# Kernel tuning notes

Hardware: AMD Instinct MI355X
Metric: run time of the kernel (lower is better)

Reference implementation:

```python
import jax, jax.numpy as jnp
import numpy as np

B, T, V, D, H, C = 128, 512, 50000, 128, 256, 10


def _lstm_scan(xs, W, U, b):
    # xs: [T, B, in]; Keras gate order i, f, g(candidate), o.
    xW = jnp.einsum('tbi,ij->tbj', xs, W) + b  # precompute input projection
    Bsz = xs.shape[1]
    Hd = U.shape[0]
    h0 = jnp.zeros((Bsz, Hd), xs.dtype)

    def step(carry, zx):
        h, c = carry
        z = zx + h @ U
        i, f, g, o = jnp.split(z, 4, axis=-1)
        i = jax.nn.sigmoid(i)
        f = jax.nn.sigmoid(f)
        g = jnp.tanh(g)
        o = jax.nn.sigmoid(o)
        c = f * c + i * g
        h = o * jnp.tanh(c)
        return (h, c), h

    (hT, _), hs = jax.lax.scan(step, (h0, h0), xW)
    return hs, hT


def setup_inputs() -> dict:
    key = jax.random.key(0)
    ks = jax.random.split(key, 16)
    f32 = jnp.float32

    def glorot(k, shape):
        fan = shape[0] + shape[1]
        return jax.random.uniform(k, shape, f32, -1.0, 1.0) * np.sqrt(6.0 / fan)

    x = jax.random.randint(ks[0], (B, T), 0, V, dtype=jnp.int32)
    emb = jax.random.normal(ks[1], (V, D), f32) * 0.05
    # layer 1: input D -> 4H per direction
    W1f = glorot(ks[2], (D, 4 * H)); U1f = glorot(ks[3], (H, 4 * H)); b1f = jnp.zeros((4 * H,), f32)
    W1b = glorot(ks[4], (D, 4 * H)); U1b = glorot(ks[5], (H, 4 * H)); b1b = jnp.zeros((4 * H,), f32)
    # layer 2: input 2H -> 4H per direction
    W2f = glorot(ks[6], (2 * H, 4 * H)); U2f = glorot(ks[7], (H, 4 * H)); b2f = jnp.zeros((4 * H,), f32)
    W2b = glorot(ks[8], (2 * H, 4 * H)); U2b = glorot(ks[9], (H, 4 * H)); b2b = jnp.zeros((4 * H,), f32)
    Wd = glorot(ks[10], (2 * H, C)); bd = jnp.zeros((C,), f32)
    return dict(x=x, emb=emb, W1f=W1f, U1f=U1f, b1f=b1f, W1b=W1b, U1b=U1b, b1b=b1b,
                W2f=W2f, U2f=U2f, b2f=b2f, W2b=W2b, U2b=U2b, b2b=b2b, Wd=Wd, bd=bd)


def reference(x, emb, W1f, U1f, b1f, W1b, U1b, b1b, W2f, U2f, b2f, W2b, U2b, b2b, Wd, bd):
    # Embedding lookup -> [T, B, D] (time-major for scan). Dropout is inference-off.
    e = jnp.transpose(emb[x], (1, 0, 2))
    # Bidirectional LSTM 1 (return_sequences)
    hs_f, _ = _lstm_scan(e, W1f, U1f, b1f)
    hs_b, _ = _lstm_scan(e[::-1], W1b, U1b, b1b)
    seq = jnp.concatenate([hs_f, hs_b[::-1]], axis=-1)  # [T, B, 2H]
    # Bidirectional LSTM 2 (return last states)
    _, hT_f = _lstm_scan(seq, W2f, U2f, b2f)
    _, hT_b = _lstm_scan(seq[::-1], W2b, U2b, b2b)
    h = jnp.concatenate([hT_f, hT_b], axis=-1)  # [B, 2H]
    return jax.nn.softmax(h @ Wd + bd, axis=-1)
```

## Files before the change

### kernel.cpp

```cpp
#include <hip/hip_runtime.h>
#include <hip/hip_bf16.h>

#define B_ 128
#define T_ 512
#define H_ 256
#define G4_ 1024
#define D_ 128

typedef short s8v   __attribute__((ext_vector_type(8)));
typedef float f32x4 __attribute__((ext_vector_type(4)));
typedef unsigned short u16x4 __attribute__((ext_vector_type(4)));
typedef unsigned short u16x8 __attribute__((ext_vector_type(8)));
typedef unsigned int   u32x4 __attribute__((ext_vector_type(4)));
typedef unsigned short ush;
typedef unsigned long long ull;

#define BAR_LDS() asm volatile("s_waitcnt lgkmcnt(0)\n\ts_barrier" ::: "memory")

__device__ __forceinline__ void xstore(ull* p, ull v) {
  (void)__hip_atomic_exchange(p, v, __ATOMIC_RELAXED, __HIP_MEMORY_SCOPE_AGENT);
}
__device__ __forceinline__ ull xload(const ull* p) {
  return __hip_atomic_load(p, __ATOMIC_RELAXED, __HIP_MEMORY_SCOPE_AGENT);
}

__device__ __align__(256) ush   g_xw[(size_t)T_ * 2 * B_ * G4_];
__device__ __align__(256) ush   g_hseq[(size_t)T_ * B_ * 512];
__device__ __align__(256) ull   g_hx2[16 * 2 * 2 * 2 * 512];
__device__ __align__(256) float g_hT[B_ * 512];
__device__ __align__(256) unsigned g_tcnt[512];
__device__ __align__(256) ush   g_wtall[2359296];

__device__ __forceinline__ ush f2b(float f) {
  unsigned u = __builtin_bit_cast(unsigned, f);
  u += 0x7FFFu + ((u >> 16) & 1u);
  return (ush)(u >> 16);
}
__device__ __forceinline__ float b2f(ush h) {
  unsigned u = ((unsigned)h) << 16;
  return __builtin_bit_cast(float, u);
}
__device__ __forceinline__ float sigm(float x) {
  x = fminf(15.f, fmaxf(-15.f, x));
  return 1.f / (1.f + __expf(-x));
}
__device__ __forceinline__ float tanh_(float x) {
  x = fminf(8.f, fmaxf(-8.f, x));
  float e = __expf(-2.f * x);
  return (1.f - e) / (1.f + e);
}

__global__ __launch_bounds__(256, 4) void prep_w(
    const float* __restrict__ Wf, const float* __restrict__ Wb,
    ush* __restrict__ WTf, ush* __restrict__ WTb, int K)
{
  __shared__ ush tile[64][65];
  const float* W = blockIdx.z ? Wb : Wf;
  ush* WT = blockIdx.z ? WTb : WTf;
  int nt = blockIdx.x & 15, kt = blockIdx.x >> 4;
  int tid = threadIdx.x;
  for (int i = tid; i < 4096; i += 256) {
    int k = i >> 6, n = i & 63;
    tile[k][n] = f2b(W[(size_t)(kt * 64 + k) * 1024 + nt * 64 + n]);
  }
  __syncthreads();
  for (int i = tid; i < 4096; i += 256) {
    int n = i >> 6, k = i & 63;
    WT[(size_t)(nt * 64 + n) * K + kt * 64 + k] = tile[k][n];
  }
}

__global__ __launch_bounds__(512, 4) void gemm_xw(
    const int* __restrict__ xi, const float* __restrict__ emb,
    const ush* __restrict__ WTf, const ush* __restrict__ WTb)
{
  __shared__ __align__(16) ush A_lds[128 * 72];
  __shared__ __align__(16) ush BT_lds[128 * 72];
  const int tid = threadIdx.x;
  const int lane = tid & 63;
  const int w = tid >> 6;
  const int nb = blockIdx.x;
  const int t = blockIdx.y;
  const int dir = blockIdx.z;
  const ush* WT = dir ? WTb : WTf;

  const f32x4 zero4 = {0.f, 0.f, 0.f, 0.f};
  f32x4 acc[8];
#pragma unroll
  for (int i = 0; i < 8; ++i) acc[i] = zero4;

  const int rowA0 = tid >> 3;
  const int ccA = tid & 7;
  int idx0 = xi[rowA0 * T_ + t];
  int idx1 = xi[(rowA0 + 64) * T_ + t];

  for (int kc = 0; kc < 2; ++kc) {
    __syncthreads();
    {
      const float* s = emb + (size_t)idx0 * D_ + kc * 64 + ccA * 8;
      f32x4 a = *(const f32x4*)s;
      f32x4 b = *(const f32x4*)(s + 4);
      u16x8 v;
      v[0]=f2b(a[0]); v[1]=f2b(a[1]); v[2]=f2b(a[2]); v[3]=f2b(a[3]);
      v[4]=f2b(b[0]); v[5]=f2b(b[1]); v[6]=f2b(b[2]); v[7]=f2b(b[3]);
      *(u16x8*)&A_lds[rowA0 * 72 + ccA * 8] = v;
    }
    {
      const float* s = emb + (size_t)idx1 * D_ + kc * 64 + ccA * 8;
      f32x4 a = *(const f32x4*)s;
      f32x4 b = *(const f32x4*)(s + 4);
      u16x8 v;
      v[0]=f2b(a[0]); v[1]=f2b(a[1]); v[2]=f2b(a[2]); v[3]=f2b(a[3]);
      v[4]=f2b(b[0]); v[5]=f2b(b[1]); v[6]=f2b(b[2]); v[7]=f2b(b[3]);
      *(u16x8*)&A_lds[(rowA0 + 64) * 72 + ccA * 8] = v;
    }
    {
      int n = tid >> 2, k8 = (tid & 3) * 2;
      const ush* src = WT + (size_t)(nb * 128 + n) * 128 + kc * 64 + k8 * 8;
      *(u32x4*)&BT_lds[n * 72 + k8 * 8] = *(const u32x4*)src;
      *(u32x4*)&BT_lds[n * 72 + k8 * 8 + 8] = *(const u32x4*)(src + 8);
    }
    __syncthreads();
#pragma unroll
    for (int kt = 0; kt < 2; ++kt) {
      const int koff = kt * 32 + ((lane >> 4) << 3);
      s8v af = *(const s8v*)&A_lds[(w * 16 + (lane & 15)) * 72 + koff];
#pragma unroll
      for (int nt = 0; nt < 8; ++nt) {
        s8v bf = *(const s8v*)&BT_lds[(nt * 16 + (lane & 15)) * 72 + koff];
        acc[nt] = __builtin_amdgcn_mfma_f32_16x16x32_bf16(af, bf, acc[nt], 0, 0, 0);
      }
    }
  }
  ush* dst = g_xw + ((size_t)t * 2 + dir) * ((size_t)B_ * G4_);
#pragma unroll
  for (int nt = 0; nt < 8; ++nt) {
    int colg = nb * 128 + nt * 16 + (lane & 15);
    int g = colg >> 8, hc = colg & 255;
#pragma unroll
    for (int jj = 0; jj < 4; ++jj) {
      int row = w * 16 + ((lane >> 4) << 2) + jj;
      dst[(size_t)row * 1024 + hc * 4 + g] = f2b(acc[nt][jj]);
    }
  }
}

__global__ __launch_bounds__(512, 2) void mega(
    int layer, const ush* __restrict__ UTf, const ush* __restrict__ UTb,
    const float* __restrict__ bfp, const float* __restrict__ bbp,
    int writeSeq, int ngemm,
    const ush* __restrict__ WT2f, const ush* __restrict__ WT2b)
{
  __shared__ __align__(16) ush smem[2 * 128 * 72];
  const int bx = blockIdx.x;
  const int tid = threadIdx.x;
  const int lane = tid & 63;
  const int w = tid >> 6;
  const int l15 = lane & 15;
  const int lq = lane >> 4;

  if (bx < 64) {
    const int slice = bx & 15;
    const int dir = (bx >> 4) & 1;
    const int nh = bx >> 5;
    const ush* UT = dir ? UTb : UTf;
    const float* bias = dir ? bbp : bfp;
    const int mycol = nh * 128 + w * 16 + l15;
    const int rowb = slice * 8;
    const unsigned sbase = (unsigned)(layer * T_);
    ush* h0 = smem;

    s8v bfr[4][8];
#pragma unroll
    for (int g = 0; g < 4; ++g) {
      const ush* up = UT + (size_t)(g * 256 + mycol) * 256;
#pragma unroll
      for (int kt = 0; kt < 8; ++kt)
        bfr[g][kt] = *(const s8v*)(up + kt * 32 + lq * 8);
    }
    float bias_r[4];
#pragma unroll
    for (int g = 0; g < 4; ++g) bias_r[g] = bias[g * 256 + mycol];

    {
      ull* z = (ull*)smem;
      z[tid] = 0ull; z[tid + 512] = 0ull; z[tid + 1024] = 0ull; z[tid + 1536] = 0ull;
    }
    __syncthreads();

    float c_[4] = {0.f, 0.f, 0.f, 0.f};
    ull* hx_sd = g_hx2 + (size_t)(slice * 2 + dir) * 2048;

    const int w_src = tid >> 6, r_ = tid & 63;
    const int blkc = r_ >> 5, lqs = (r_ >> 4) & 1, l15s = r_ & 15;
    const int col_p = (nh ^ 1) * 128 + w_src * 16 + l15s;
    const int r0c = lqs * 4 + blkc * 2;
    const int c8p = col_p >> 3, wp = col_p & 7;
    const int sw0 = ((c8p ^ r0c) & 31) * 8 + wp;
    const int sw1 = ((c8p ^ (r0c + 1)) & 31) * 8 + wp;
    const int xrow = (lq & 1) * 4;

    u16x4 xv[4];
    {
      int t0 = dir ? (T_ - 1) : 0;
      const ush* xp = g_xw + (((size_t)t0 * 2 + dir) * B_ + rowb) * 1024 + mycol * 4;
#pragma unroll
      for (int j = 0; j < 4; ++j) xv[j] = *(const u16x4*)(xp + (size_t)(xrow + j) * 1024);
    }

    for (int s = 0; s < T_; ++s) {
      const int p = s & 1;
      if (s > 0) {
        const ull* ap = hx_sd + (size_t)(p * 2 + (nh ^ 1)) * 512 + tid;
        unsigned target = sbase + (unsigned)s;
        ull v;
        for (;;) {
          v = xload(ap);
          if ((unsigned)(v >> 32) >= target) break;
          __builtin_amdgcn_s_sleep(1);
        }
        ush* dl = h0 + p * 4096;
        dl[r0c * 256 + sw0] = (ush)v;
        dl[(r0c + 1) * 256 + sw1] = (ush)(v >> 16);
      }
      BAR_LDS();
      if (writeSeq) {
        if (tid == 0 && s >= 2) {
          int td = dir ? (T_ + 1 - s) : (s - 2);
          __hip_atomic_fetch_add(&g_tcnt[td], 1u, __ATOMIC_RELAXED, __HIP_MEMORY_SCOPE_AGENT);
        }
        if (s > 0 && tid < 128) {
          int row8 = tid >> 4, idx = tid & 15;
          int col = nh * 128 + idx * 8;
          int c8 = col >> 3;
          const ush* srcl = h0 + p * 4096 + row8 * 256 + ((c8 ^ row8) & 31) * 8;
          ull lo = *(const ull*)srcl;
          ull hi = *(const ull*)(srcl + 4);
          int tprev = dir ? (T_ - s) : (s - 1);
          ull* dst = (ull*)&g_hseq[((size_t)tprev * B_ + rowb + row8) * 512 + dir * 256 + col];
          xstore(dst, lo);
          xstore(dst + 1, hi);
        }
      }
      u16x4 xn[4];
      {
        int tn = dir ? max(0, T_ - 2 - s) : min(T_ - 1, s + 1);
        const ush* xp = g_xw + (((size_t)tn * 2 + dir) * B_ + rowb) * 1024 + mycol * 4;
#pragma unroll
        for (int j = 0; j < 4; ++j) xn[j] = *(const u16x4*)(xp + (size_t)(xrow + j) * 1024);
      }
      s8v af[8];
#pragma unroll
      for (int kt = 0; kt < 8; ++kt) {
        int c8 = kt * 4 + lq;
        af[kt] = *(const s8v*)(h0 + p * 4096 + l15 * 256 + ((c8 ^ l15) & 31) * 8);
      }
      f32x4 acc[4];
      const f32x4 zero4 = {0.f, 0.f, 0.f, 0.f};
#pragma unroll
      for (int g = 0; g < 4; ++g) acc[g] = zero4;
#pragma unroll
      for (int kt = 0; kt < 8; ++kt) {
#pragma unroll
        for (int g = 0; g < 4; ++g)
          acc[g] = __builtin_amdgcn_mfma_f32_16x16x32_bf16(af[kt], bfr[g][kt], acc[g], 0, 0, 0);
      }
      ush hv[4];
#pragma unroll
      for (int j = 0; j < 4; ++j) {
        float vi = acc[0][j] + b2f(xv[j][0]) + bias_r[0];
        float vf = acc[1][j] + b2f(xv[j][1]) + bias_r[1];
        float vg = acc[2][j] + b2f(xv[j][2]) + bias_r[2];
        float vo = acc[3][j] + b2f(xv[j][3]) + bias_r[3];
        float ig = sigm(vi), fg = sigm(vf), gg = tanh_(vg), og = sigm(vo);
        float cc = fg * c_[j] + ig * gg;
        c_[j] = cc;
        hv[j] = f2b(og * tanh_(cc));
      }
      if (lq < 2 && s + 1 < T_) {
        ull seqw = ((ull)(sbase + (unsigned)s + 1u)) << 32;
        ull e0 = (ull)hv[0] | ((ull)hv[1] << 16) | seqw;
        ull e1 = (ull)hv[2] | ((ull)hv[3] << 16) | seqw;
        ull* ep = hx_sd + (size_t)((p ^ 1) * 2 + nh) * 512 + w * 64 + lq * 16 + l15;
        xstore(ep, e0);
        xstore(ep + 32, e1);
      }
      if (lq < 2) {
        int c8o = mycol >> 3, wo = mycol & 7;
        ush* dl = h0 + (p ^ 1) * 4096;
#pragma unroll
        for (int j = 0; j < 4; ++j) {
          int r = lq * 4 + j;
          dl[r * 256 + (((c8o ^ r) & 31) * 8 + wo)] = hv[j];
        }
      }
#pragma unroll
      for (int j = 0; j < 4; ++j) xv[j] = xn[j];
    }
    __syncthreads();
    const ush* bufl = h0 + (T_ & 1) * 4096;
    if (writeSeq) {
      if (tid < 128) {
        int row8 = tid >> 4, idx = tid & 15;
        int col = nh * 128 + idx * 8;
        int c8 = col >> 3;
        const ush* srcl = bufl + row8 * 256 + ((c8 ^ row8) & 31) * 8;
        ull lo = *(const ull*)srcl;
        ull hi = *(const ull*)(srcl + 4);
        int tlast = dir ? 0 : (T_ - 1);
        ull* dst = (ull*)&g_hseq[((size_t)tlast * B_ + rowb + row8) * 512 + dir * 256 + col];
        xstore(dst, lo);
        xstore(dst + 1, hi);
      }
      asm volatile("s_waitcnt vmcnt(0)" ::: "memory");
      __syncthreads();
      if (tid == 0) {
        int ta = dir ? 1 : (T_ - 2);
        int tb2 = dir ? 0 : (T_ - 1);
        __hip_atomic_fetch_add(&g_tcnt[ta], 1u, __ATOMIC_RELAXED, __HIP_MEMORY_SCOPE_AGENT);
        __hip_atomic_fetch_add(&g_tcnt[tb2], 1u, __ATOMIC_RELAXED, __HIP_MEMORY_SCOPE_AGENT);
      }
    } else {
      if (tid < 128) {
        int row8 = tid >> 4, idx = tid & 15;
        int col = nh * 128 + idx * 8;
        int c8 = col >> 3;
        const ush* srcl = bufl + row8 * 256 + ((c8 ^ row8) & 31) * 8;
        float* dstf = g_hT + (size_t)(rowb + row8) * 512 + dir * 256 + col;
        f32x4 f0, f1;
#pragma unroll
        for (int j = 0; j < 4; ++j) { f0[j] = b2f(srcl[j]); f1[j] = b2f(srcl[4 + j]); }
        *(f32x4*)dstf = f0;
        *(f32x4*)(dstf + 4) = f1;
      }
    }
  } else {
    if (ngemm <= 0) return;
    ush* A_lds = smem;
    ush* BT_lds = smem + 128 * 72;
    const int wg = bx - 64;
    const int rowA0 = tid >> 3;
    const int ccA = tid & 7;

    for (int u = wg; u < 8192; u += ngemm) {
      int pairIdx = u >> 4, sub = u & 15;
      int nb = sub & 7, gdir = sub >> 3;
      int t = (pairIdx & 1) ? (255 - (pairIdx >> 1)) : (256 + (pairIdx >> 1));
      const ush* WT = gdir ? WT2b : WT2f;
      for (;;) {
        unsigned v = __hip_atomic_load(&g_tcnt[t], __ATOMIC_RELAXED, __HIP_MEMORY_SCOPE_AGENT);
        if (v >= 64u) break;
        __builtin_amdgcn_s_sleep(4);
      }
      const f32x4 zero4 = {0.f, 0.f, 0.f, 0.f};
      f32x4 acc[8];
#pragma unroll
      for (int i = 0; i < 8; ++i) acc[i] = zero4;
      for (int kc = 0; kc < 8; ++kc) {
        __syncthreads();
        {
          const ush* s0 = g_hseq + ((size_t)(t * B_ + rowA0)) * 512 + kc * 64 + ccA * 8;
          *(u32x4*)&A_lds[rowA0 * 72 + ccA * 8] = *(const u32x4*)s0;
          const ush* s1 = g_hseq + ((size_t)(t * B_ + rowA0 + 64)) * 512 + kc * 64 + ccA * 8;
          *(u32x4*)&A_lds[(rowA0 + 64) * 72 + ccA * 8] = *(const u32x4*)s1;
        }
        {
          int n = tid >> 2, k8 = (tid & 3) * 2;
          const ush* src = WT + (size_t)(nb * 128 + n) * 512 + kc * 64 + k8 * 8;
          *(u32x4*)&BT_lds[n * 72 + k8 * 8] = *(const u32x4*)src;
          *(u32x4*)&BT_lds[n * 72 + k8 * 8 + 8] = *(const u32x4*)(src + 8);
        }
        __syncthreads();
#pragma unroll
        for (int kt = 0; kt < 2; ++kt) {
          const int koff = kt * 32 + (lq << 3);
          s8v af = *(const s8v*)&A_lds[(w * 16 + l15) * 72 + koff];
#pragma unroll
          for (int nt = 0; nt < 8; ++nt) {
            s8v bf = *(const s8v*)&BT_lds[(nt * 16 + l15) * 72 + koff];
            acc[nt] = __builtin_amdgcn_mfma_f32_16x16x32_bf16(af, bf, acc[nt], 0, 0, 0);
          }
        }
      }
      ush* dst = g_xw + ((size_t)t * 2 + gdir) * ((size_t)B_ * G4_);
#pragma unroll
      for (int nt = 0; nt < 8; ++nt) {
        int colg = nb * 128 + nt * 16 + l15;
        int g = colg >> 8, hc = colg & 255;
#pragma unroll
        for (int jj = 0; jj < 4; ++jj) {
          int row = w * 16 + (lq << 2) + jj;
          dst[(size_t)row * 1024 + hc * 4 + g] = f2b(acc[nt][jj]);
        }
      }
    }
  }
}

__global__ __launch_bounds__(512, 1) void dense_softmax(
    const float* __restrict__ Wd, const float* __restrict__ bd, float* __restrict__ out)
{
  __shared__ float wT[10 * 512];
  __shared__ float part[512 * 10];
  int tid = threadIdx.x;
  for (int i = tid; i < 5120; i += 512) {
    int k = i / 10, j = i - k * 10;
    wT[j * 512 + k] = Wd[i];
  }
  __syncthreads();
  int row = tid >> 2, q = tid & 3;
  float acc[10];
#pragma unroll
  for (int j = 0; j < 10; ++j) acc[j] = 0.f;
  const float* hrow = g_hT + (size_t)row * 512 + q * 128;
  for (int kk = 0; kk < 32; ++kk) {
    f32x4 h4 = *(const f32x4*)(hrow + kk * 4);
#pragma unroll
    for (int j = 0; j < 10; ++j) {
      f32x4 w4 = *(const f32x4*)&wT[j * 512 + q * 128 + kk * 4];
      acc[j] += h4[0] * w4[0] + h4[1] * w4[1] + h4[2] * w4[2] + h4[3] * w4[3];
    }
  }
#pragma unroll
  for (int j = 0; j < 10; ++j) part[tid * 10 + j] = acc[j];
  __syncthreads();
  if (tid < 128) {
    float lg[10];
#pragma unroll
    for (int j = 0; j < 10; ++j)
      lg[j] = bd[j] + part[(tid * 4 + 0) * 10 + j] + part[(tid * 4 + 1) * 10 + j]
                    + part[(tid * 4 + 2) * 10 + j] + part[(tid * 4 + 3) * 10 + j];
    float m = lg[0];
#pragma unroll
    for (int j = 1; j < 10; ++j) m = fmaxf(m, lg[j]);
    float ssum = 0.f;
#pragma unroll
    for (int j = 0; j < 10; ++j) { lg[j] = __expf(lg[j] - m); ssum += lg[j]; }
    float inv = 1.f / ssum;
#pragma unroll
    for (int j = 0; j < 10; ++j) out[tid * 10 + j] = lg[j] * inv;
  }
}

extern "C" void kernel_launch(void* const* d_in, const int* in_sizes, int n_in,
                              void* d_out, int out_size, void* d_ws, size_t ws_size,
                              hipStream_t stream) {
  (void)in_sizes; (void)n_in; (void)d_ws; (void)ws_size; (void)out_size;
  const int* x = (const int*)d_in[0];
  const float* emb = (const float*)d_in[1];
  const float* W1f = (const float*)d_in[2];
  const float* U1f = (const float*)d_in[3];
  const float* b1f = (const float*)d_in[4];
  const float* W1b = (const float*)d_in[5];
  const float* U1b = (const float*)d_in[6];
  const float* b1b = (const float*)d_in[7];
  const float* W2f = (const float*)d_in[8];
  const float* U2f = (const float*)d_in[9];
  const float* b2f = (const float*)d_in[10];
  const float* W2b = (const float*)d_in[11];
  const float* U2b = (const float*)d_in[12];
  const float* b2b = (const float*)d_in[13];
  const float* Wd  = (const float*)d_in[14];
  const float* bd  = (const float*)d_in[15];
  float* out = (float*)d_out;

  void* hx_p = nullptr; void* wt_p = nullptr; void* tc_p = nullptr;
  hipGetSymbolAddress(&hx_p, HIP_SYMBOL(g_hx2));
  hipGetSymbolAddress(&wt_p, HIP_SYMBOL(g_wtall));
  hipGetSymbolAddress(&tc_p, HIP_SYMBOL(g_tcnt));
  ush* wt = (ush*)wt_p;
  hipMemsetAsync(hx_p, 0, sizeof(ull) * 16 * 2 * 2 * 2 * 512, stream);
  hipMemsetAsync(tc_p, 0, sizeof(unsigned) * 512, stream);

  ush* wt1f = wt;                 ush* wt1b = wt1f + 131072;
  ush* ut1f = wt1b + 131072;      ush* ut1b = ut1f + 262144;
  ush* wt2f = ut1b + 262144;      ush* wt2b = wt2f + 524288;
  ush* ut2f = wt2b + 524288;      ush* ut2b = ut2f + 262144;

  prep_w<<<dim3(32, 1, 2), 256, 0, stream>>>(W1f, W1b, wt1f, wt1b, 128);
  prep_w<<<dim3(64, 1, 2), 256, 0, stream>>>(U1f, U1b, ut1f, ut1b, 256);
  prep_w<<<dim3(128, 1, 2), 256, 0, stream>>>(W2f, W2b, wt2f, wt2b, 512);
  prep_w<<<dim3(64, 1, 2), 256, 0, stream>>>(U2f, U2b, ut2f, ut2b, 256);

  gemm_xw<<<dim3(8, T_, 2), 512, 0, stream>>>(x, emb, wt1f, wt1b);
  mega<<<256, 512, 0, stream>>>(0, ut1f, ut1b, b1f, b1b, 1, 192, wt2f, wt2b);
  mega<<<64, 512, 0, stream>>>(1, ut2f, ut2b, b2f, b2b, 0, 0, nullptr, nullptr);
  dense_softmax<<<1, 512, 0, stream>>>(Wd, bd, out);
}
```

Measured before the change: 3.308 ms.

## Split recurrent matmul into own-half and partner-half to overlap with exchange

The recurrent h@U product is split by K into the half this block computed itself and the half owned by the partner block. The own-half MFMAs are issued right after the new h is written to LDS, before waiting on the partner's data, so only the partner-half remains on the critical path after the cross-block spin-wait. The next-step xW prefetch is also moved to after the gate computation. This adds an extra LDS barrier per step, and the accumulators now carry across iterations.

```diff
diff --git a/kernel.cpp b/kernel.cpp
--- a/kernel.cpp
+++ b/kernel.cpp
@@ -170,13 +170,15 @@
     const unsigned sbase = (unsigned)(layer * T_);
     ush* h0 = smem;
 
-    s8v bfr[4][8];
+    s8v bfrO[4][4], bfrP[4][4];
 #pragma unroll
     for (int g = 0; g < 4; ++g) {
       const ush* up = UT + (size_t)(g * 256 + mycol) * 256;
 #pragma unroll
-      for (int kt = 0; kt < 8; ++kt)
-        bfr[g][kt] = *(const s8v*)(up + kt * 32 + lq * 8);
+      for (int i = 0; i < 4; ++i) {
+        bfrO[g][i] = *(const s8v*)(up + (nh * 128 + i * 32) + lq * 8);
+        bfrP[g][i] = *(const s8v*)(up + ((nh ^ 1) * 128 + i * 32) + lq * 8);
+      }
     }
     float bias_r[4];
 #pragma unroll
@@ -207,6 +209,11 @@
 #pragma unroll
       for (int j = 0; j < 4; ++j) xv[j] = *(const u16x4*)(xp + (size_t)(xrow + j) * 1024);
     }
+
+    const f32x4 zero4 = {0.f, 0.f, 0.f, 0.f};
+    f32x4 acc[4];
+#pragma unroll
+    for (int g = 0; g < 4; ++g) acc[g] = zero4;
 
     for (int s = 0; s < T_; ++s) {
       const int p = s & 1;
@@ -242,28 +249,19 @@
           xstore(dst + 1, hi);
         }
       }
-      u16x4 xn[4];
       {
-        int tn = dir ? max(0, T_ - 2 - s) : min(T_ - 1, s + 1);
-        const ush* xp = g_xw + (((size_t)tn * 2 + dir) * B_ + rowb) * 1024 + mycol * 4;
-#pragma unroll
-        for (int j = 0; j < 4; ++j) xn[j] = *(const u16x4*)(xp + (size_t)(xrow + j) * 1024);
-      }
-      s8v af[8];
-#pragma unroll
-      for (int kt = 0; kt < 8; ++kt) {
-        int c8 = kt * 4 + lq;
-        af[kt] = *(const s8v*)(h0 + p * 4096 + l15 * 256 + ((c8 ^ l15) & 31) * 8);
-      }
-      f32x4 acc[4];
-      const f32x4 zero4 = {0.f, 0.f, 0.f, 0.f};
-#pragma unroll
-      for (int g = 0; g < 4; ++g) acc[g] = zero4;
-#pragma unroll
-      for (int kt = 0; kt < 8; ++kt) {
-#pragma unroll
-        for (int g = 0; g < 4; ++g)
-          acc[g] = __builtin_amdgcn_mfma_f32_16x16x32_bf16(af[kt], bfr[g][kt], acc[g], 0, 0, 0);
+        s8v afP[4];
+#pragma unroll
+        for (int i = 0; i < 4; ++i) {
+          int c8 = ((nh ^ 1) * 4 + i) * 4 + lq;
+          afP[i] = *(const s8v*)(h0 + p * 4096 + l15 * 256 + ((c8 ^ l15) & 31) * 8);
+        }
+#pragma unroll
+        for (int i = 0; i < 4; ++i) {
+#pragma unroll
+          for (int g = 0; g < 4; ++g)
+            acc[g] = __builtin_amdgcn_mfma_f32_16x16x32_bf16(afP[i], bfrP[g][i], acc[g], 0, 0, 0);
+        }
       }
       ush hv[4];
 #pragma unroll
@@ -277,6 +275,13 @@
         c_[j] = cc;
         hv[j] = f2b(og * tanh_(cc));
       }
+      u16x4 xn[4];
+      {
+        int tn = dir ? max(0, T_ - 2 - s) : min(T_ - 1, s + 1);
+        const ush* xp = g_xw + (((size_t)tn * 2 + dir) * B_ + rowb) * 1024 + mycol * 4;
+#pragma unroll
+        for (int j = 0; j < 4; ++j) xn[j] = *(const u16x4*)(xp + (size_t)(xrow + j) * 1024);
+      }
       if (lq < 2 && s + 1 < T_) {
         ull seqw = ((ull)(sbase + (unsigned)s + 1u)) << 32;
         ull e0 = (ull)hv[0] | ((ull)hv[1] << 16) | seqw;
@@ -292,6 +297,23 @@
         for (int j = 0; j < 4; ++j) {
           int r = lq * 4 + j;
           dl[r * 256 + (((c8o ^ r) & 31) * 8 + wo)] = hv[j];
+        }
+      }
+      BAR_LDS();
+#pragma unroll
+      for (int g = 0; g < 4; ++g) acc[g] = zero4;
+      {
+        s8v afO[4];
+#pragma unroll
+        for (int i = 0; i < 4; ++i) {
+          int c8 = (nh * 4 + i) * 4 + lq;
+          afO[i] = *(const s8v*)(h0 + (p ^ 1) * 4096 + l15 * 256 + ((c8 ^ l15) & 31) * 8);
+        }
+#pragma unroll
+        for (int i = 0; i < 4; ++i) {
+#pragma unroll
+          for (int g = 0; g < 4; ++g)
+            acc[g] = __builtin_amdgcn_mfma_f32_16x16x32_bf16(afO[i], bfrO[g][i], acc[g], 0, 0, 0);
         }
       }
 #pragma unroll
```

After: 3.244 ms. Within noise of the previous version (-1.9%).

## Give each recurrent block all 256 hidden columns to drop cross-block h exchange

Applied to the files above, without the earlier changes.

Recurrent blocks now use 1024 threads (16 waves) and each one owns every hidden column for 16 batch rows, so the per-step hidden state is exchanged through LDS with a single barrier. The global-memory spin-wait handshake between paired blocks and the g_hx2 buffer are removed. Blocks per layer drop from 64 to 16, the hseq writeout and completion counters are adjusted to match (pipelined one step later with a vmcnt wait), and the overlapped layer-2 input GEMM blocks are re-tiled for 16 waves. In exchange, each block holds twice the recurrent work serially, so fewer CUs run the recurrence and per-step latency may grow.

```diff
diff --git a/kernel.cpp b/kernel.cpp
--- a/kernel.cpp
+++ b/kernel.cpp
@@ -18,15 +18,11 @@
 #define BAR_LDS() asm volatile("s_waitcnt lgkmcnt(0)\n\ts_barrier" ::: "memory")
 
 __device__ __forceinline__ void xstore(ull* p, ull v) {
-  (void)__hip_atomic_exchange(p, v, __ATOMIC_RELAXED, __HIP_MEMORY_SCOPE_AGENT);
-}
-__device__ __forceinline__ ull xload(const ull* p) {
-  return __hip_atomic_load(p, __ATOMIC_RELAXED, __HIP_MEMORY_SCOPE_AGENT);
+  __hip_atomic_store(p, v, __ATOMIC_RELAXED, __HIP_MEMORY_SCOPE_AGENT);
 }
 
 __device__ __align__(256) ush   g_xw[(size_t)T_ * 2 * B_ * G4_];
 __device__ __align__(256) ush   g_hseq[(size_t)T_ * B_ * 512];
-__device__ __align__(256) ull   g_hx2[16 * 2 * 2 * 2 * 512];
 __device__ __align__(256) float g_hT[B_ * 512];
 __device__ __align__(256) unsigned g_tcnt[512];
 __device__ __align__(256) ush   g_wtall[2359296];
@@ -145,7 +141,7 @@
   }
 }
 
-__global__ __launch_bounds__(512, 2) void mega(
+__global__ __launch_bounds__(1024, 1) void mega(
     int layer, const ush* __restrict__ UTf, const ush* __restrict__ UTb,
     const float* __restrict__ bfp, const float* __restrict__ bbp,
     int writeSeq, int ngemm,
@@ -159,15 +155,13 @@
   const int l15 = lane & 15;
   const int lq = lane >> 4;
 
-  if (bx < 64) {
-    const int slice = bx & 15;
-    const int dir = (bx >> 4) & 1;
-    const int nh = bx >> 5;
+  if (bx < 16) {
+    const int slice = bx & 7;
+    const int dir = bx >> 3;
     const ush* UT = dir ? UTb : UTf;
     const float* bias = dir ? bbp : bfp;
-    const int mycol = nh * 128 + w * 16 + l15;
-    const int rowb = slice * 8;
-    const unsigned sbase = (unsigned)(layer * T_);
+    const int mycol = w * 16 + l15;
+    const int rowb = slice * 16;
     ush* h0 = smem;
 
     s8v bfr[4][8];
@@ -184,62 +178,40 @@
 
     {
       ull* z = (ull*)smem;
-      z[tid] = 0ull; z[tid + 512] = 0ull; z[tid + 1024] = 0ull; z[tid + 1536] = 0ull;
+      z[tid] = 0ull; z[tid + 1024] = 0ull;
     }
     __syncthreads();
 
     float c_[4] = {0.f, 0.f, 0.f, 0.f};
-    ull* hx_sd = g_hx2 + (size_t)(slice * 2 + dir) * 2048;
-
-    const int w_src = tid >> 6, r_ = tid & 63;
-    const int blkc = r_ >> 5, lqs = (r_ >> 4) & 1, l15s = r_ & 15;
-    const int col_p = (nh ^ 1) * 128 + w_src * 16 + l15s;
-    const int r0c = lqs * 4 + blkc * 2;
-    const int c8p = col_p >> 3, wp = col_p & 7;
-    const int sw0 = ((c8p ^ r0c) & 31) * 8 + wp;
-    const int sw1 = ((c8p ^ (r0c + 1)) & 31) * 8 + wp;
-    const int xrow = (lq & 1) * 4;
+
+    const int srow = tid >> 6;
+    const int scg = tid & 63;
+    const int sc8 = scg >> 1, swo = (scg & 1) * 4;
+    const int sswz = ((sc8 ^ srow) & 31) * 8 + swo;
 
     u16x4 xv[4];
     {
       int t0 = dir ? (T_ - 1) : 0;
       const ush* xp = g_xw + (((size_t)t0 * 2 + dir) * B_ + rowb) * 1024 + mycol * 4;
 #pragma unroll
-      for (int j = 0; j < 4; ++j) xv[j] = *(const u16x4*)(xp + (size_t)(xrow + j) * 1024);
-    }
+      for (int j = 0; j < 4; ++j) xv[j] = *(const u16x4*)(xp + (size_t)(lq * 4 + j) * 1024);
+    }
+
+    const f32x4 zero4 = {0.f, 0.f, 0.f, 0.f};
 
     for (int s = 0; s < T_; ++s) {
       const int p = s & 1;
-      if (s > 0) {
-        const ull* ap = hx_sd + (size_t)(p * 2 + (nh ^ 1)) * 512 + tid;
-        unsigned target = sbase + (unsigned)s;
-        ull v;
-        for (;;) {
-          v = xload(ap);
-          if ((unsigned)(v >> 32) >= target) break;
-          __builtin_amdgcn_s_sleep(1);
-        }
-        ush* dl = h0 + p * 4096;
-        dl[r0c * 256 + sw0] = (ush)v;
-        dl[(r0c + 1) * 256 + sw1] = (ush)(v >> 16);
-      }
-      BAR_LDS();
       if (writeSeq) {
-        if (tid == 0 && s >= 2) {
-          int td = dir ? (T_ + 1 - s) : (s - 2);
+        asm volatile("s_waitcnt vmcnt(0)" ::: "memory");
+        if (tid == 0 && s >= 3) {
+          int td = dir ? (T_ + 2 - s) : (s - 3);
           __hip_atomic_fetch_add(&g_tcnt[td], 1u, __ATOMIC_RELAXED, __HIP_MEMORY_SCOPE_AGENT);
         }
-        if (s > 0 && tid < 128) {
-          int row8 = tid >> 4, idx = tid & 15;
-          int col = nh * 128 + idx * 8;
-          int c8 = col >> 3;
-          const ush* srcl = h0 + p * 4096 + row8 * 256 + ((c8 ^ row8) & 31) * 8;
-          ull lo = *(const ull*)srcl;
-          ull hi = *(const ull*)(srcl + 4);
+        if (s > 0) {
+          const ush* srcl = h0 + p * 4096 + srow * 256 + sswz;
           int tprev = dir ? (T_ - s) : (s - 1);
-          ull* dst = (ull*)&g_hseq[((size_t)tprev * B_ + rowb + row8) * 512 + dir * 256 + col];
-          xstore(dst, lo);
-          xstore(dst + 1, hi);
+          xstore((ull*)&g_hseq[((size_t)tprev * B_ + rowb + srow) * 512 + dir * 256 + scg * 4],
+                 *(const ull*)srcl);
         }
       }
       u16x4 xn[4];
@@ -247,7 +219,7 @@
         int tn = dir ? max(0, T_ - 2 - s) : min(T_ - 1, s + 1);
         const ush* xp = g_xw + (((size_t)tn * 2 + dir) * B_ + rowb) * 1024 + mycol * 4;
 #pragma unroll
-        for (int j = 0; j < 4; ++j) xn[j] = *(const u16x4*)(xp + (size_t)(xrow + j) * 1024);
+        for (int j = 0; j < 4; ++j) xn[j] = *(const u16x4*)(xp + (size_t)(lq * 4 + j) * 1024);
       }
       s8v af[8];
 #pragma unroll
@@ -256,7 +228,6 @@
         af[kt] = *(const s8v*)(h0 + p * 4096 + l15 * 256 + ((c8 ^ l15) & 31) * 8);
       }
       f32x4 acc[4];
-      const f32x4 zero4 = {0.f, 0.f, 0.f, 0.f};
 #pragma unroll
       for (int g = 0; g < 4; ++g) acc[g] = zero4;
 #pragma unroll
@@ -277,15 +248,7 @@
         c_[j] = cc;
         hv[j] = f2b(og * tanh_(cc));
       }
-      if (lq < 2 && s + 1 < T_) {
-        ull seqw = ((ull)(sbase + (unsigned)s + 1u)) << 32;
-        ull e0 = (ull)hv[0] | ((ull)hv[1] << 16) | seqw;
-        ull e1 = (ull)hv[2] | ((ull)hv[3] << 16) | seqw;
-        ull* ep = hx_sd + (size_t)((p ^ 1) * 2 + nh) * 512 + w * 64 + lq * 16 + l15;
-        xstore(ep, e0);
-        xstore(ep + 32, e1);
-      }
-      if (lq < 2) {
+      {
         int c8o = mycol >> 3, wo = mycol & 7;
         ush* dl = h0 + (p ^ 1) * 4096;
 #pragma unroll
@@ -294,53 +257,45 @@
           dl[r * 256 + (((c8o ^ r) & 31) * 8 + wo)] = hv[j];
         }
       }
+      BAR_LDS();
 #pragma unroll
       for (int j = 0; j < 4; ++j) xv[j] = xn[j];
     }
-    __syncthreads();
     const ush* bufl = h0 + (T_ & 1) * 4096;
     if (writeSeq) {
-      if (tid < 128) {
-        int row8 = tid >> 4, idx = tid & 15;
-        int col = nh * 128 + idx * 8;
-        int c8 = col >> 3;
-        const ush* srcl = bufl + row8 * 256 + ((c8 ^ row8) & 31) * 8;
-        ull lo = *(const ull*)srcl;
-        ull hi = *(const ull*)(srcl + 4);
+      {
+        const ush* srcl = bufl + srow * 256 + sswz;
         int tlast = dir ? 0 : (T_ - 1);
-        ull* dst = (ull*)&g_hseq[((size_t)tlast * B_ + rowb + row8) * 512 + dir * 256 + col];
-        xstore(dst, lo);
-        xstore(dst + 1, hi);
+        xstore((ull*)&g_hseq[((size_t)tlast * B_ + rowb + srow) * 512 + dir * 256 + scg * 4],
+               *(const ull*)srcl);
       }
       asm volatile("s_waitcnt vmcnt(0)" ::: "memory");
       __syncthreads();
       if (tid == 0) {
-        int ta = dir ? 1 : (T_ - 2);
-        int tb2 = dir ? 0 : (T_ - 1);
+        int ta = dir ? 2 : (T_ - 3);
+        int tb = dir ? 1 : (T_ - 2);
+        int tc = dir ? 0 : (T_ - 1);
         __hip_atomic_fetch_add(&g_tcnt[ta], 1u, __ATOMIC_RELAXED, __HIP_MEMORY_SCOPE_AGENT);
-        __hip_atomic_fetch_add(&g_tcnt[tb2], 1u, __ATOMIC_RELAXED, __HIP_MEMORY_SCOPE_AGENT);
+        __hip_atomic_fetch_add(&g_tcnt[tb], 1u, __ATOMIC_RELAXED, __HIP_MEMORY_SCOPE_AGENT);
+        __hip_atomic_fetch_add(&g_tcnt[tc], 1u, __ATOMIC_RELAXED, __HIP_MEMORY_SCOPE_AGENT);
       }
     } else {
-      if (tid < 128) {
-        int row8 = tid >> 4, idx = tid & 15;
-        int col = nh * 128 + idx * 8;
-        int c8 = col >> 3;
-        const ush* srcl = bufl + row8 * 256 + ((c8 ^ row8) & 31) * 8;
-        float* dstf = g_hT + (size_t)(rowb + row8) * 512 + dir * 256 + col;
-        f32x4 f0, f1;
-#pragma unroll
-        for (int j = 0; j < 4; ++j) { f0[j] = b2f(srcl[j]); f1[j] = b2f(srcl[4 + j]); }
-        *(f32x4*)dstf = f0;
-        *(f32x4*)(dstf + 4) = f1;
-      }
+      const ush* srcl = bufl + srow * 256 + sswz;
+      float* dstf = g_hT + (size_t)(rowb + srow) * 512 + dir * 256 + scg * 4;
+      f32x4 fv;
+#pragma unroll
+      for (int j = 0; j < 4; ++j) fv[j] = b2f(srcl[j]);
+      *(f32x4*)dstf = fv;
     }
   } else {
     if (ngemm <= 0) return;
     ush* A_lds = smem;
     ush* BT_lds = smem + 128 * 72;
-    const int wg = bx - 64;
-    const int rowA0 = tid >> 3;
+    const int wg = bx - 16;
+    const int rowA = tid >> 3;
     const int ccA = tid & 7;
+    const int rs = w & 7;
+    const int ch = w >> 3;
 
     for (int u = wg; u < 8192; u += ngemm) {
       int pairIdx = u >> 4, sub = u & 15;
@@ -349,47 +304,41 @@
       const ush* WT = gdir ? WT2b : WT2f;
       for (;;) {
         unsigned v = __hip_atomic_load(&g_tcnt[t], __ATOMIC_RELAXED, __HIP_MEMORY_SCOPE_AGENT);
-        if (v >= 64u) break;
+        if (v >= 16u) break;
         __builtin_amdgcn_s_sleep(4);
       }
       const f32x4 zero4 = {0.f, 0.f, 0.f, 0.f};
-      f32x4 acc[8];
-#pragma unroll
-      for (int i = 0; i < 8; ++i) acc[i] = zero4;
+      f32x4 acc[4];
+#pragma unroll
+      for (int i = 0; i < 4; ++i) acc[i] = zero4;
       for (int kc = 0; kc < 8; ++kc) {
         __syncthreads();
         {
-          const ush* s0 = g_hseq + ((size_t)(t * B_ + rowA0)) * 512 + kc * 64 + ccA * 8;
-          *(u32x4*)&A_lds[rowA0 * 72 + ccA * 8] = *(const u32x4*)s0;
-          const ush* s1 = g_hseq + ((size_t)(t * B_ + rowA0 + 64)) * 512 + kc * 64 + ccA * 8;
-          *(u32x4*)&A_lds[(rowA0 + 64) * 72 + ccA * 8] = *(const u32x4*)s1;
-        }
-        {
-          int n = tid >> 2, k8 = (tid & 3) * 2;
-          const ush* src = WT + (size_t)(nb * 128 + n) * 512 + kc * 64 + k8 * 8;
-          *(u32x4*)&BT_lds[n * 72 + k8 * 8] = *(const u32x4*)src;
-          *(u32x4*)&BT_lds[n * 72 + k8 * 8 + 8] = *(const u32x4*)(src + 8);
+          const ush* s0 = g_hseq + ((size_t)(t * B_ + rowA)) * 512 + kc * 64 + ccA * 8;
+          *(u32x4*)&A_lds[rowA * 72 + ccA * 8] = *(const u32x4*)s0;
+          const ush* s1 = WT + (size_t)(nb * 128 + rowA) * 512 + kc * 64 + ccA * 8;
+          *(u32x4*)&BT_lds[rowA * 72 + ccA * 8] = *(const u32x4*)s1;
         }
         __syncthreads();
 #pragma unroll
         for (int kt = 0; kt < 2; ++kt) {
           const int koff = kt * 32 + (lq << 3);
-          s8v af = *(const s8v*)&A_lds[(w * 16 + l15) * 72 + koff];
-#pragma unroll
-          for (int nt = 0; nt < 8; ++nt) {
-            s8v bf = *(const s8v*)&BT_lds[(nt * 16 + l15) * 72 + koff];
+          s8v af = *(const s8v*)&A_lds[(rs * 16 + l15) * 72 + koff];
+#pragma unroll
+          for (int nt = 0; nt < 4; ++nt) {
+            s8v bf = *(const s8v*)&BT_lds[(ch * 64 + nt * 16 + l15) * 72 + koff];
             acc[nt] = __builtin_amdgcn_mfma_f32_16x16x32_bf16(af, bf, acc[nt], 0, 0, 0);
           }
         }
       }
       ush* dst = g_xw + ((size_t)t * 2 + gdir) * ((size_t)B_ * G4_);
 #pragma unroll
-      for (int nt = 0; nt < 8; ++nt) {
-        int colg = nb * 128 + nt * 16 + l15;
+      for (int nt = 0; nt < 4; ++nt) {
+        int colg = nb * 128 + ch * 64 + nt * 16 + l15;
         int g = colg >> 8, hc = colg & 255;
 #pragma unroll
         for (int jj = 0; jj < 4; ++jj) {
-          int row = w * 16 + (lq << 2) + jj;
+          int row = rs * 16 + (lq << 2) + jj;
           dst[(size_t)row * 1024 + hc * 4 + g] = f2b(acc[nt][jj]);
         }
       }
@@ -464,12 +413,10 @@
   const float* bd  = (const float*)d_in[15];
   float* out = (float*)d_out;
 
-  void* hx_p = nullptr; void* wt_p = nullptr; void* tc_p = nullptr;
-  hipGetSymbolAddress(&hx_p, HIP_SYMBOL(g_hx2));
+  void* wt_p = nullptr; void* tc_p = nullptr;
   hipGetSymbolAddress(&wt_p, HIP_SYMBOL(g_wtall));
   hipGetSymbolAddress(&tc_p, HIP_SYMBOL(g_tcnt));
   ush* wt = (ush*)wt_p;
-  hipMemsetAsync(hx_p, 0, sizeof(ull) * 16 * 2 * 2 * 2 * 512, stream);
   hipMemsetAsync(tc_p, 0, sizeof(unsigned) * 512, stream);
 
   ush* wt1f = wt;                 ush* wt1b = wt1f + 131072;
@@ -483,7 +430,7 @@
   prep_w<<<dim3(64, 1, 2), 256, 0, stream>>>(U2f, U2b, ut2f, ut2b, 256);
 
   gemm_xw<<<dim3(8, T_, 2), 512, 0, stream>>>(x, emb, wt1f, wt1b);
-  mega<<<256, 512, 0, stream>>>(0, ut1f, ut1b, b1f, b1b, 1, 192, wt2f, wt2b);
-  mega<<<64, 512, 0, stream>>>(1, ut2f, ut2b, b2f, b2b, 0, 0, nullptr, nullptr);
+  mega<<<208, 1024, 0, stream>>>(0, ut1f, ut1b, b1f, b1b, 1, 192, wt2f, wt2b);
+  mega<<<16, 1024, 0, stream>>>(1, ut2f, ut2b, b2f, b2b, 0, 0, nullptr, nullptr);
   dense_softmax<<<1, 512, 0, stream>>>(Wd, bd, out);
 }
```

Result: slower. 11.23 ms (+239.5%).
